# Performance work log

Measured on AMD Instinct MI355X. Metric: run time of the kernel, lower is better.

Reference implementation:

```python
import jax, jax.numpy as jnp
import numpy as np

N = 32768       # flattened residues (batch*seq)
DIM = 1024      # dim == channel (required by residual add)
NRES = 21       # amino-acid types
RECYCLES = 2


def _quat_to_rot(q):
    w, x, y, z = q[..., 0], q[..., 1], q[..., 2], q[..., 3]
    return jnp.stack([
        jnp.stack([1 - 2 * (y * y + z * z), 2 * (x * y - w * z), 2 * (x * z + w * y)], -1),
        jnp.stack([2 * (x * y + w * z), 1 - 2 * (x * x + z * z), 2 * (y * z - w * x)], -1),
        jnp.stack([2 * (x * z - w * y), 2 * (y * z + w * x), 1 - 2 * (x * x + y * y)], -1),
    ], -2)


def _rand_rigid(key, shape, tscale=1.0):
    # random valid rigid transforms as 4x4 homogeneous matrices
    kq, kt = jax.random.split(key)
    q = jax.random.normal(kq, shape + (4,), jnp.float32)
    q = q / jnp.linalg.norm(q, axis=-1, keepdims=True)
    rot = _quat_to_rot(q)
    t = jax.random.normal(kt, shape + (3,), jnp.float32) * tscale
    m = jnp.zeros(shape + (4, 4), jnp.float32)
    m = m.at[..., :3, :3].set(rot).at[..., :3, 3].set(t).at[..., 3, 3].set(1.0)
    return m


def setup_inputs():
    key = jax.random.key(0)
    ks = jax.random.split(key, 12)
    s = 1.0 / np.sqrt(DIM)
    return {
        "rep0": jax.random.normal(ks[0], (N, DIM), jnp.float32),
        "rep1": jax.random.normal(ks[1], (N, DIM), jnp.float32),
        "w_in": jax.random.normal(ks[2], (DIM, DIM), jnp.float32) * s,
        "b_in": jnp.zeros((DIM,), jnp.float32),
        "w1": jax.random.normal(ks[3], (DIM, DIM), jnp.float32) * s,
        "b1": jnp.zeros((DIM,), jnp.float32),
        "w2": jax.random.normal(ks[4], (DIM, DIM), jnp.float32) * s,
        "b2": jnp.zeros((DIM,), jnp.float32),
        "w_ang": jax.random.normal(ks[5], (DIM, 14), jnp.float32) * s,
        "b_ang": jnp.zeros((14,), jnp.float32),
        "rigids": _rand_rigid(ks[6], (N,), tscale=10.0),              # backbone frames
        "default_frames": _rand_rigid(ks[7], (NRES, 8), tscale=1.5), # restype_rigid_group_default_frame
        "lit_positions": jax.random.normal(ks[8], (NRES, 14, 3), jnp.float32),
        "atom_mask": (jax.random.uniform(ks[9], (NRES, 14)) > 0.2).astype(jnp.float32),
        "aatype": jax.random.randint(ks[10], (N,), 0, NRES),
        "group_idx": jax.random.randint(ks[11], (NRES, 14), 0, 8),   # restype_atom14_to_rigid_group
    }


def reference(rep0, rep1, w_in, b_in, w1, b1, w2, b2, w_ang, b_ang,
              rigids, default_frames, lit_positions, atom_mask, aatype, group_idx):
    # InputProjection: shared ReLU+Linear applied to each representation, summed
    act = (jax.nn.relu(rep0) @ w_in + b_in) + (jax.nn.relu(rep1) @ w_in + b_in)
    # ResidueBlock with residual recycles: act += Linear(ReLU(Linear(ReLU(act))))
    for _ in range(RECYCLES):
        h = jax.nn.relu(act) @ w1 + b1
        h = jax.nn.relu(h) @ w2 + b2
        act = act + h
    # TorisonAngles: Linear(dim,14) -> (N,7,2) -> l2_normalize
    ang = (jax.nn.relu(act) @ w_ang + b_ang).reshape(N, 7, 2)
    angles = ang / jnp.sqrt(jnp.maximum(jnp.sum(ang * ang, -1, keepdims=True), 1e-12))
    # torsion_angles_to_frames: prepend identity backbone angle (sin=0, cos=1)
    sin = jnp.concatenate([jnp.zeros((N, 1), angles.dtype), angles[..., 0]], 1)  # [N,8]
    cos = jnp.concatenate([jnp.ones((N, 1), angles.dtype), angles[..., 1]], 1)
    z = jnp.zeros_like(sin); one = jnp.ones_like(sin)
    rotx = jnp.stack([
        jnp.stack([one, z, z, z], -1),
        jnp.stack([z, cos, -sin, z], -1),
        jnp.stack([z, sin, cos, z], -1),
        jnp.stack([z, z, z, one], -1),
    ], -2)                                            # [N,8,4,4] rotation about x by torsion
    frames = default_frames[aatype] @ rotx            # [N,8,4,4]
    # chi2/chi3/chi4 frames are defined relative to the previous chi frame
    f5 = frames[:, 4] @ frames[:, 5]
    f6 = f5 @ frames[:, 6]
    f7 = f6 @ frames[:, 7]
    frames_to_bb = jnp.concatenate([frames[:, :5], jnp.stack([f5, f6, f7], 1)], 1)
    frames_global = rigids[:, None] @ frames_to_bb    # [N,8,4,4]
    # frames_and_literature_positions_to_atom14_pos
    gidx = group_idx[aatype]                          # [N,14] rigid-group id per atom
    f14 = jnp.take_along_axis(frames_global,
                              jnp.broadcast_to(gidx[:, :, None, None], (N, 14, 4, 4)),
                              axis=1)                 # [N,14,4,4]
    pos = lit_positions[aatype]                       # [N,14,3]
    pred = jnp.einsum('naij,naj->nai', f14[..., :3, :3], pos) + f14[..., :3, 3]
    pred = pred * atom_mask[aatype][..., None]        # [N,14,3]
    return angles, pred, frames_global
```

## Files before the change

kernel.cpp:

```cpp
#include <hip/hip_runtime.h>
#include <stdint.h>

typedef uint16_t u16;
typedef uint32_t u32;
typedef __bf16 bf16;
typedef bf16 bf16x8 __attribute__((ext_vector_type(8)));
typedef float f32x4 __attribute__((ext_vector_type(4)));

#define N_RES 32768
#define DIM 1024

__device__ __forceinline__ float b2f(u16 u) {
  u32 v = ((u32)u) << 16;
  float f;
  __builtin_memcpy(&f, &v, 4);
  return f;
}
__device__ __forceinline__ u16 f2b(float f) {
  u32 u;
  __builtin_memcpy(&u, &f, 4);
  u += 0x7fffu + ((u >> 16) & 1u);
  return (u16)(u >> 16);
}
__device__ __forceinline__ void split2(float v, u16& h, u16& l) {
  h = f2b(v);
  l = f2b(v - b2f(h));
}
__device__ __forceinline__ void relu_mask4(uint4& h, uint4& l) {
  u32 s, m;
  s = h.x & 0x80008000u; m = ((s >> 15) & 0x00010001u) * 0xFFFFu; h.x &= ~m; l.x &= ~m;
  s = h.y & 0x80008000u; m = ((s >> 15) & 0x00010001u) * 0xFFFFu; h.y &= ~m; l.y &= ~m;
  s = h.z & 0x80008000u; m = ((s >> 15) & 0x00010001u) * 0xFFFFu; h.z &= ~m; l.z &= ~m;
  s = h.w & 0x80008000u; m = ((s >> 15) & 0x00010001u) * 0xFFFFu; h.w &= ~m; l.w &= ~m;
}
__device__ __forceinline__ void relu_split8(bf16x8& h, bf16x8& l) {
  uint4 uh, ul;
  __builtin_memcpy(&uh, &h, 16);
  __builtin_memcpy(&ul, &l, 16);
  relu_mask4(uh, ul);
  __builtin_memcpy(&h, &uh, 16);
  __builtin_memcpy(&l, &ul, 16);
}
__device__ __forceinline__ void split8(const float* v, uint4& H, uint4& L) {
  u16 h[8], l[8];
#pragma unroll
  for (int i = 0; i < 8; ++i) split2(v[i], h[i], l[i]);
  H.x = (u32)h[0] | ((u32)h[1] << 16);
  H.y = (u32)h[2] | ((u32)h[3] << 16);
  H.z = (u32)h[4] | ((u32)h[5] << 16);
  H.w = (u32)h[6] | ((u32)h[7] << 16);
  L.x = (u32)l[0] | ((u32)l[1] << 16);
  L.y = (u32)l[2] | ((u32)l[3] << 16);
  L.z = (u32)l[4] | ((u32)l[5] << 16);
  L.w = (u32)l[6] | ((u32)l[7] << 16);
}

__global__ __launch_bounds__(256) void transpose_split(const float* __restrict__ in,
                                                       u16* __restrict__ outh,
                                                       u16* __restrict__ outl) {
  __shared__ float t[32][33];
  const int bx = blockIdx.x * 32, by = blockIdx.y * 32;
  const int tx = threadIdx.x, ty = threadIdx.y;
  for (int i = ty; i < 32; i += 8) t[i][tx] = in[(size_t)(by + i) * DIM + bx + tx];
  __syncthreads();
  for (int i = ty; i < 32; i += 8) {
    u16 h, l;
    split2(t[tx][i], h, l);
    const size_t o = (size_t)(bx + i) * DIM + by + tx;
    outh[o] = h;
    outl[o] = l;
  }
}

__global__ __launch_bounds__(256, 2) void gemm_split(
    const u16* __restrict__ Ah, const u16* __restrict__ Al, int reluA,
    const float* __restrict__ repA0, const float* __restrict__ repA1,
    const u16* __restrict__ Bh, const u16* __restrict__ Bl,
    const float* __restrict__ bias, float bscale,
    const u16* __restrict__ Rh, const u16* __restrict__ Rl,
    u16* __restrict__ Oh, u16* __restrict__ Ol) {
  __shared__ __align__(16) u16 Ash[128 * 32];
  __shared__ __align__(16) u16 Asl[128 * 32];
  __shared__ __align__(16) u16 Bsh[128 * 32];
  __shared__ __align__(16) u16 Bsl[128 * 32];
  const int tid = threadIdx.x;
  const int wave = tid >> 6;
  const int lane = tid & 63;
  const int lrow = lane & 15;
  const int lquad = lane >> 4;
  const int bm = blockIdx.y * 128;
  const int bn = blockIdx.x * 128;
  const int wm = (wave & 1) * 64;
  const int wn = (wave >> 1) * 64;

  f32x4 acc[4][4];
#pragma unroll
  for (int i = 0; i < 4; ++i)
#pragma unroll
    for (int j = 0; j < 4; ++j) acc[i][j] = (f32x4){0.f, 0.f, 0.f, 0.f};

  for (int kb = 0; kb < DIM; kb += 32) {
#pragma unroll
    for (int q = 0; q < 2; ++q) {
      const int idx = q * 256 + tid;
      const int r = idx >> 2;
      const int c = idx & 3;
      const size_t goA = (size_t)(bm + r) * DIM + kb + c * 8;
      const size_t goB = (size_t)(bn + r) * DIM + kb + c * 8;
      uint4 ah, al;
      if (repA0) {
        float4 x0 = *(const float4*)(repA0 + goA);
        float4 x1 = *(const float4*)(repA0 + goA + 4);
        float4 y0 = *(const float4*)(repA1 + goA);
        float4 y1 = *(const float4*)(repA1 + goA + 4);
        float v[8];
        v[0] = fmaxf(x0.x, 0.f) + fmaxf(y0.x, 0.f);
        v[1] = fmaxf(x0.y, 0.f) + fmaxf(y0.y, 0.f);
        v[2] = fmaxf(x0.z, 0.f) + fmaxf(y0.z, 0.f);
        v[3] = fmaxf(x0.w, 0.f) + fmaxf(y0.w, 0.f);
        v[4] = fmaxf(x1.x, 0.f) + fmaxf(y1.x, 0.f);
        v[5] = fmaxf(x1.y, 0.f) + fmaxf(y1.y, 0.f);
        v[6] = fmaxf(x1.z, 0.f) + fmaxf(y1.z, 0.f);
        v[7] = fmaxf(x1.w, 0.f) + fmaxf(y1.w, 0.f);
        split8(v, ah, al);
      } else {
        ah = *(const uint4*)(Ah + goA);
        al = *(const uint4*)(Al + goA);
        if (reluA) relu_mask4(ah, al);
      }
      uint4 bh = *(const uint4*)(Bh + goB);
      uint4 bl = *(const uint4*)(Bl + goB);
      *(uint4*)(Ash + r * 32 + c * 8) = ah;
      *(uint4*)(Asl + r * 32 + c * 8) = al;
      *(uint4*)(Bsh + r * 32 + c * 8) = bh;
      *(uint4*)(Bsl + r * 32 + c * 8) = bl;
    }
    __syncthreads();
    bf16x8 a_h[4], a_l[4], b_h[4], b_l[4];
#pragma unroll
    for (int i = 0; i < 4; ++i) {
      a_h[i] = *(const bf16x8*)(Ash + (wm + i * 16 + lrow) * 32 + lquad * 8);
      a_l[i] = *(const bf16x8*)(Asl + (wm + i * 16 + lrow) * 32 + lquad * 8);
    }
#pragma unroll
    for (int j = 0; j < 4; ++j) {
      b_h[j] = *(const bf16x8*)(Bsh + (wn + j * 16 + lrow) * 32 + lquad * 8);
      b_l[j] = *(const bf16x8*)(Bsl + (wn + j * 16 + lrow) * 32 + lquad * 8);
    }
#pragma unroll
    for (int i = 0; i < 4; ++i)
#pragma unroll
      for (int j = 0; j < 4; ++j) {
        acc[i][j] = __builtin_amdgcn_mfma_f32_16x16x32_bf16(a_h[i], b_h[j], acc[i][j], 0, 0, 0);
        acc[i][j] = __builtin_amdgcn_mfma_f32_16x16x32_bf16(a_h[i], b_l[j], acc[i][j], 0, 0, 0);
        acc[i][j] = __builtin_amdgcn_mfma_f32_16x16x32_bf16(a_l[i], b_h[j], acc[i][j], 0, 0, 0);
      }
    __syncthreads();
  }

#pragma unroll
  for (int j = 0; j < 4; ++j) {
    const int col = bn + wn + j * 16 + lrow;
    const float bj = bias[col] * bscale;
#pragma unroll
    for (int i = 0; i < 4; ++i) {
      const int row0 = bm + wm + i * 16 + lquad * 4;
#pragma unroll
      for (int r = 0; r < 4; ++r) {
        const size_t idx = (size_t)(row0 + r) * DIM + col;
        float v = acc[i][j][r] + bj;
        if (Rh) v += b2f(Rh[idx]) + b2f(Rl[idx]);
        u16 h, l;
        split2(v, h, l);
        Oh[idx] = h;
        Ol[idx] = l;
      }
    }
  }
}

__global__ __launch_bounds__(256) void angles_split(
    const u16* __restrict__ ACTh, const u16* __restrict__ ACTl,
    const u16* __restrict__ WAh, const u16* __restrict__ WAl,
    const float* __restrict__ b_ang, float* __restrict__ out_angles) {
  const int tid = threadIdx.x;
  const int wave = tid >> 6, lane = tid & 63;
  const int lrow = lane & 15, lquad = lane >> 4;
  const int rowA = blockIdx.x * 64 + wave * 16 + lrow;
  f32x4 acc = (f32x4){0.f, 0.f, 0.f, 0.f};
  const u16* gah = ACTh + (size_t)rowA * DIM + lquad * 8;
  const u16* gal = ACTl + (size_t)rowA * DIM + lquad * 8;
  const u16* gbh = WAh + (size_t)lrow * DIM + lquad * 8;
  const u16* gbl = WAl + (size_t)lrow * DIM + lquad * 8;
#pragma unroll 4
  for (int kb = 0; kb < DIM; kb += 32) {
    bf16x8 ah = *(const bf16x8*)(gah + kb);
    bf16x8 al = *(const bf16x8*)(gal + kb);
    relu_split8(ah, al);
    bf16x8 bh = *(const bf16x8*)(gbh + kb);
    bf16x8 bl = *(const bf16x8*)(gbl + kb);
    acc = __builtin_amdgcn_mfma_f32_16x16x32_bf16(ah, bh, acc, 0, 0, 0);
    acc = __builtin_amdgcn_mfma_f32_16x16x32_bf16(ah, bl, acc, 0, 0, 0);
    acc = __builtin_amdgcn_mfma_f32_16x16x32_bf16(al, bh, acc, 0, 0, 0);
  }
  const int col = lrow;
  const float bj = (col < 14) ? b_ang[col] : 0.f;
#pragma unroll
  for (int r = 0; r < 4; ++r) {
    float v = acc[r] + bj;
    float p = __shfl_xor(v, 1, 64);
    float s2 = fmaxf(v * v + p * p, 1e-12f);
    float o = v * rsqrtf(s2);
    const int orow = blockIdx.x * 64 + wave * 16 + lquad * 4 + r;
    if (col < 14) out_angles[(size_t)orow * 14 + col] = o;
  }
}

__global__ __launch_bounds__(256) void prep_wang(const float* __restrict__ w,
                                                 u16* __restrict__ outh,
                                                 u16* __restrict__ outl) {
  for (int idx = threadIdx.x; idx < 16 * 1024; idx += 256) {
    const int n = idx & 15;
    const int k = idx >> 4;
    const float v = (n < 14) ? w[(size_t)k * 14 + n] : 0.f;
    u16 h, l;
    split2(v, h, l);
    outh[(size_t)n * DIM + k] = h;
    outl[(size_t)n * DIM + k] = l;
  }
}

__device__ __forceinline__ void mm34(const float* A, const float* B, float* O) {
#pragma unroll
  for (int r = 0; r < 3; ++r) {
#pragma unroll
    for (int c = 0; c < 4; ++c) {
      float v = A[r * 4 + 0] * B[0 * 4 + c] + A[r * 4 + 1] * B[1 * 4 + c] +
                A[r * 4 + 2] * B[2 * 4 + c];
      if (c == 3) v += A[r * 4 + 3];
      O[r * 4 + c] = v;
    }
  }
}

__global__ __launch_bounds__(256) void frames_kernel(
    const float* __restrict__ angles, const float* __restrict__ rigids,
    const float* __restrict__ dframes, const float* __restrict__ litpos,
    const float* __restrict__ amask, const int* __restrict__ aatype,
    const int* __restrict__ gidx, float* __restrict__ out_pred,
    float* __restrict__ out_frames) {
  const int n = blockIdx.x * 256 + threadIdx.x;
  const int aa = aatype[n];

  float fr[8][12];
  const float* angp = angles + (size_t)n * 14;
#pragma unroll
  for (int g = 0; g < 8; ++g) {
    float s, c;
    if (g == 0) { s = 0.f; c = 1.f; }
    else { s = angp[(g - 1) * 2]; c = angp[(g - 1) * 2 + 1]; }
    const float* D = dframes + ((size_t)aa * 8 + g) * 16;
#pragma unroll
    for (int r = 0; r < 3; ++r) {
      float d0 = D[r * 4 + 0], d1 = D[r * 4 + 1], d2 = D[r * 4 + 2], d3 = D[r * 4 + 3];
      fr[g][r * 4 + 0] = d0;
      fr[g][r * 4 + 1] = d1 * c + d2 * s;
      fr[g][r * 4 + 2] = d2 * c - d1 * s;
      fr[g][r * 4 + 3] = d3;
    }
  }
  float tmp[12];
  mm34(fr[4], fr[5], tmp);
#pragma unroll
  for (int e = 0; e < 12; ++e) fr[5][e] = tmp[e];
  mm34(fr[5], fr[6], tmp);
#pragma unroll
  for (int e = 0; e < 12; ++e) fr[6][e] = tmp[e];
  mm34(fr[6], fr[7], tmp);
#pragma unroll
  for (int e = 0; e < 12; ++e) fr[7][e] = tmp[e];

  float R[12];
  const float* rp = rigids + (size_t)n * 16;
#pragma unroll
  for (int e = 0; e < 12; ++e) R[e] = rp[e];
#pragma unroll
  for (int g = 0; g < 8; ++g) {
    mm34(R, fr[g], tmp);
#pragma unroll
    for (int e = 0; e < 12; ++e) fr[g][e] = tmp[e];
  }

  float4* of = (float4*)(out_frames + (size_t)n * 128);
#pragma unroll
  for (int g = 0; g < 8; ++g) {
    of[g * 4 + 0] = (float4){fr[g][0], fr[g][1], fr[g][2], fr[g][3]};
    of[g * 4 + 1] = (float4){fr[g][4], fr[g][5], fr[g][6], fr[g][7]};
    of[g * 4 + 2] = (float4){fr[g][8], fr[g][9], fr[g][10], fr[g][11]};
    of[g * 4 + 3] = (float4){0.f, 0.f, 0.f, 1.f};
  }

  float P[42];
#pragma unroll
  for (int a = 0; a < 14; ++a) {
    const int g = gidx[aa * 14 + a];
    float f[12];
#pragma unroll
    for (int q = 0; q < 8; ++q) {
      if (q == 0) {
#pragma unroll
        for (int e = 0; e < 12; ++e) f[e] = fr[0][e];
      } else {
        const bool sel = (g == q);
#pragma unroll
        for (int e = 0; e < 12; ++e) f[e] = sel ? fr[q][e] : f[e];
      }
    }
    const float px = litpos[((size_t)aa * 14 + a) * 3 + 0];
    const float py = litpos[((size_t)aa * 14 + a) * 3 + 1];
    const float pz = litpos[((size_t)aa * 14 + a) * 3 + 2];
    const float mk = amask[aa * 14 + a];
    P[a * 3 + 0] = (f[0] * px + f[1] * py + f[2] * pz + f[3]) * mk;
    P[a * 3 + 1] = (f[4] * px + f[5] * py + f[6] * pz + f[7]) * mk;
    P[a * 3 + 2] = (f[8] * px + f[9] * py + f[10] * pz + f[11]) * mk;
  }
  float2* op = (float2*)(out_pred + (size_t)n * 42);
#pragma unroll
  for (int i = 0; i < 21; ++i) op[i] = (float2){P[2 * i], P[2 * i + 1]};
}

__global__ __launch_bounds__(256) void ws_diag(float* __restrict__ out, float mb) {
  const int i = blockIdx.x * 256 + threadIdx.x;
  if (i < N_RES * 14) out[i] = mb;
}

extern "C" void kernel_launch(void* const* d_in, const int* in_sizes, int n_in,
                              void* d_out, int out_size, void* d_ws, size_t ws_size,
                              hipStream_t stream) {
  const float* rep0 = (const float*)d_in[0];
  const float* rep1 = (const float*)d_in[1];
  const float* w_in = (const float*)d_in[2];
  const float* b_in = (const float*)d_in[3];
  const float* w1 = (const float*)d_in[4];
  const float* b1 = (const float*)d_in[5];
  const float* w2 = (const float*)d_in[6];
  const float* b2 = (const float*)d_in[7];
  const float* w_ang = (const float*)d_in[8];
  const float* b_ang = (const float*)d_in[9];
  const float* rigids = (const float*)d_in[10];
  const float* dframes = (const float*)d_in[11];
  const float* litpos = (const float*)d_in[12];
  const float* amask = (const float*)d_in[13];
  const int* aatype = (const int*)d_in[14];
  const int* gidx = (const int*)d_in[15];

  const size_t SLOT = (size_t)N_RES * DIM;
  const size_t NEED_U16 = 4 * SLOT + 6 * (size_t)DIM * DIM + 2 * 16 * DIM;

  float* out_ang = (float*)d_out;
  float* out_pred = out_ang + (size_t)N_RES * 14;
  float* out_frames = out_pred + (size_t)N_RES * 42;

  if (ws_size < NEED_U16 * 2) {
    ws_diag<<<(N_RES * 14 + 255) / 256, 256, 0, stream>>>(
        out_ang, (float)(ws_size >> 20));
    return;
  }

  u16* ACTh = (u16*)d_ws;
  u16* ACTl = ACTh + SLOT;
  u16* Hh = ACTl + SLOT;
  u16* Hl = Hh + SLOT;
  u16* W0h = Hl + SLOT;
  u16* W0l = W0h + (size_t)DIM * DIM;
  u16* W1h = W0l + (size_t)DIM * DIM;
  u16* W1l = W1h + (size_t)DIM * DIM;
  u16* W2h = W1l + (size_t)DIM * DIM;
  u16* W2l = W2h + (size_t)DIM * DIM;
  u16* WAh = W2l + (size_t)DIM * DIM;
  u16* WAl = WAh + (size_t)16 * DIM;

  transpose_split<<<dim3(32, 32), dim3(32, 8), 0, stream>>>(w_in, W0h, W0l);
  transpose_split<<<dim3(32, 32), dim3(32, 8), 0, stream>>>(w1, W1h, W1l);
  transpose_split<<<dim3(32, 32), dim3(32, 8), 0, stream>>>(w2, W2h, W2l);
  prep_wang<<<1, 256, 0, stream>>>(w_ang, WAh, WAl);

  dim3 gg(DIM / 128, N_RES / 128);
  gemm_split<<<gg, 256, 0, stream>>>(nullptr, nullptr, 0, rep0, rep1,
                                     W0h, W0l, b_in, 2.f, nullptr, nullptr,
                                     ACTh, ACTl);
  gemm_split<<<gg, 256, 0, stream>>>(ACTh, ACTl, 1, nullptr, nullptr,
                                     W1h, W1l, b1, 1.f, nullptr, nullptr,
                                     Hh, Hl);
  gemm_split<<<gg, 256, 0, stream>>>(Hh, Hl, 1, nullptr, nullptr,
                                     W2h, W2l, b2, 1.f, ACTh, ACTl,
                                     ACTh, ACTl);
  gemm_split<<<gg, 256, 0, stream>>>(ACTh, ACTl, 1, nullptr, nullptr,
                                     W1h, W1l, b1, 1.f, nullptr, nullptr,
                                     Hh, Hl);
  gemm_split<<<gg, 256, 0, stream>>>(Hh, Hl, 1, nullptr, nullptr,
                                     W2h, W2l, b2, 1.f, ACTh, ACTl,
                                     ACTh, ACTl);

  angles_split<<<N_RES / 64, 256, 0, stream>>>(ACTh, ACTl, WAh, WAl, b_ang,
                                               out_ang);
  frames_kernel<<<N_RES / 256, 256, 0, stream>>>(out_ang, rigids, dframes, litpos,
                                                 amask, aatype, gidx, out_pred,
                                                 out_frames);
}
```

Measured before the change: 1.920 ms.

## Load GEMM tiles via global_load_lds, precompute input split, remap blocks per XCD

Moves the first-layer input preprocessing (relu-sum and hi/lo bf16 split) into a separate elementwise kernel so every GEMM takes pre-split bf16 operands. The GEMM tile loads now use direct global-to-LDS DMA (global_load_lds), skipping VGPR staging, and the ReLU mask is applied after reading fragments from LDS. Block indices are remapped so each XCD handles a contiguous band of row tiles, which should improve L2 reuse of A rows and B. The cost is one extra pass over the input activations and ReLU work repeated on every fragment read, with no double buffering.

```diff
diff --git a/kernel.cpp b/kernel.cpp
--- a/kernel.cpp
+++ b/kernel.cpp
@@ -53,6 +53,12 @@
   L.y = (u32)l[2] | ((u32)l[3] << 16);
   L.z = (u32)l[4] | ((u32)l[5] << 16);
   L.w = (u32)l[6] | ((u32)l[7] << 16);
+}
+
+__device__ __forceinline__ void g2l16(const void* g, void* lds) {
+  __builtin_amdgcn_global_load_lds(
+      (__attribute__((address_space(1))) void*)(g),
+      (__attribute__((address_space(3))) void*)(lds), 16, 0, 0);
 }
 
 __global__ __launch_bounds__(256) void transpose_split(const float* __restrict__ in,
@@ -72,9 +78,32 @@
   }
 }
 
+__global__ __launch_bounds__(256) void prep_input(const float* __restrict__ rep0,
+                                                  const float* __restrict__ rep1,
+                                                  u16* __restrict__ oh,
+                                                  u16* __restrict__ ol) {
+  const size_t base = ((size_t)blockIdx.x * 256 + threadIdx.x) * 8;
+  float4 x0 = *(const float4*)(rep0 + base);
+  float4 x1 = *(const float4*)(rep0 + base + 4);
+  float4 y0 = *(const float4*)(rep1 + base);
+  float4 y1 = *(const float4*)(rep1 + base + 4);
+  float v[8];
+  v[0] = fmaxf(x0.x, 0.f) + fmaxf(y0.x, 0.f);
+  v[1] = fmaxf(x0.y, 0.f) + fmaxf(y0.y, 0.f);
+  v[2] = fmaxf(x0.z, 0.f) + fmaxf(y0.z, 0.f);
+  v[3] = fmaxf(x0.w, 0.f) + fmaxf(y0.w, 0.f);
+  v[4] = fmaxf(x1.x, 0.f) + fmaxf(y1.x, 0.f);
+  v[5] = fmaxf(x1.y, 0.f) + fmaxf(y1.y, 0.f);
+  v[6] = fmaxf(x1.z, 0.f) + fmaxf(y1.z, 0.f);
+  v[7] = fmaxf(x1.w, 0.f) + fmaxf(y1.w, 0.f);
+  uint4 H, L;
+  split8(v, H, L);
+  *(uint4*)(oh + base) = H;
+  *(uint4*)(ol + base) = L;
+}
+
 __global__ __launch_bounds__(256, 2) void gemm_split(
     const u16* __restrict__ Ah, const u16* __restrict__ Al, int reluA,
-    const float* __restrict__ repA0, const float* __restrict__ repA1,
     const u16* __restrict__ Bh, const u16* __restrict__ Bl,
     const float* __restrict__ bias, float bscale,
     const u16* __restrict__ Rh, const u16* __restrict__ Rl,
@@ -88,8 +117,13 @@
   const int lane = tid & 63;
   const int lrow = lane & 15;
   const int lquad = lane >> 4;
-  const int bm = blockIdx.y * 128;
-  const int bn = blockIdx.x * 128;
+
+  const int g = blockIdx.x + (blockIdx.y << 3);
+  const int xcd = g & 7;
+  const int j = g >> 3;
+  const int bm = (xcd * 32 + (j >> 3)) * 128;
+  const int bn = (j & 7) * 128;
+
   const int wm = (wave & 1) * 64;
   const int wn = (wave >> 1) * 64;
 
@@ -97,70 +131,64 @@
 #pragma unroll
   for (int i = 0; i < 4; ++i)
 #pragma unroll
-    for (int j = 0; j < 4; ++j) acc[i][j] = (f32x4){0.f, 0.f, 0.f, 0.f};
+    for (int jj = 0; jj < 4; ++jj) acc[i][jj] = (f32x4){0.f, 0.f, 0.f, 0.f};
+
+  const int r0 = tid >> 2;
+  const int c0 = tid & 3;
+  const u16* pAh0 = Ah + (size_t)(bm + r0) * DIM + c0 * 8;
+  const u16* pAh1 = Ah + (size_t)(bm + 64 + r0) * DIM + c0 * 8;
+  const u16* pAl0 = Al + (size_t)(bm + r0) * DIM + c0 * 8;
+  const u16* pAl1 = Al + (size_t)(bm + 64 + r0) * DIM + c0 * 8;
+  const u16* pBh0 = Bh + (size_t)(bn + r0) * DIM + c0 * 8;
+  const u16* pBh1 = Bh + (size_t)(bn + 64 + r0) * DIM + c0 * 8;
+  const u16* pBl0 = Bl + (size_t)(bn + r0) * DIM + c0 * 8;
+  const u16* pBl1 = Bl + (size_t)(bn + 64 + r0) * DIM + c0 * 8;
+  u16* dA0 = Ash + (size_t)tid * 8;
+  u16* dA1 = Ash + (size_t)(tid + 256) * 8;
+  u16* dAl0 = Asl + (size_t)tid * 8;
+  u16* dAl1 = Asl + (size_t)(tid + 256) * 8;
+  u16* dB0 = Bsh + (size_t)tid * 8;
+  u16* dB1 = Bsh + (size_t)(tid + 256) * 8;
+  u16* dBl0 = Bsl + (size_t)tid * 8;
+  u16* dBl1 = Bsl + (size_t)(tid + 256) * 8;
 
   for (int kb = 0; kb < DIM; kb += 32) {
-#pragma unroll
-    for (int q = 0; q < 2; ++q) {
-      const int idx = q * 256 + tid;
-      const int r = idx >> 2;
-      const int c = idx & 3;
-      const size_t goA = (size_t)(bm + r) * DIM + kb + c * 8;
-      const size_t goB = (size_t)(bn + r) * DIM + kb + c * 8;
-      uint4 ah, al;
-      if (repA0) {
-        float4 x0 = *(const float4*)(repA0 + goA);
-        float4 x1 = *(const float4*)(repA0 + goA + 4);
-        float4 y0 = *(const float4*)(repA1 + goA);
-        float4 y1 = *(const float4*)(repA1 + goA + 4);
-        float v[8];
-        v[0] = fmaxf(x0.x, 0.f) + fmaxf(y0.x, 0.f);
-        v[1] = fmaxf(x0.y, 0.f) + fmaxf(y0.y, 0.f);
-        v[2] = fmaxf(x0.z, 0.f) + fmaxf(y0.z, 0.f);
-        v[3] = fmaxf(x0.w, 0.f) + fmaxf(y0.w, 0.f);
-        v[4] = fmaxf(x1.x, 0.f) + fmaxf(y1.x, 0.f);
-        v[5] = fmaxf(x1.y, 0.f) + fmaxf(y1.y, 0.f);
-        v[6] = fmaxf(x1.z, 0.f) + fmaxf(y1.z, 0.f);
-        v[7] = fmaxf(x1.w, 0.f) + fmaxf(y1.w, 0.f);
-        split8(v, ah, al);
-      } else {
-        ah = *(const uint4*)(Ah + goA);
-        al = *(const uint4*)(Al + goA);
-        if (reluA) relu_mask4(ah, al);
-      }
-      uint4 bh = *(const uint4*)(Bh + goB);
-      uint4 bl = *(const uint4*)(Bl + goB);
-      *(uint4*)(Ash + r * 32 + c * 8) = ah;
-      *(uint4*)(Asl + r * 32 + c * 8) = al;
-      *(uint4*)(Bsh + r * 32 + c * 8) = bh;
-      *(uint4*)(Bsl + r * 32 + c * 8) = bl;
-    }
+    g2l16(pAh0 + kb, dA0);
+    g2l16(pAh1 + kb, dA1);
+    g2l16(pAl0 + kb, dAl0);
+    g2l16(pAl1 + kb, dAl1);
+    g2l16(pBh0 + kb, dB0);
+    g2l16(pBh1 + kb, dB1);
+    g2l16(pBl0 + kb, dBl0);
+    g2l16(pBl1 + kb, dBl1);
     __syncthreads();
+
     bf16x8 a_h[4], a_l[4], b_h[4], b_l[4];
 #pragma unroll
     for (int i = 0; i < 4; ++i) {
       a_h[i] = *(const bf16x8*)(Ash + (wm + i * 16 + lrow) * 32 + lquad * 8);
       a_l[i] = *(const bf16x8*)(Asl + (wm + i * 16 + lrow) * 32 + lquad * 8);
-    }
-#pragma unroll
-    for (int j = 0; j < 4; ++j) {
-      b_h[j] = *(const bf16x8*)(Bsh + (wn + j * 16 + lrow) * 32 + lquad * 8);
-      b_l[j] = *(const bf16x8*)(Bsl + (wn + j * 16 + lrow) * 32 + lquad * 8);
+      if (reluA) relu_split8(a_h[i], a_l[i]);
+    }
+#pragma unroll
+    for (int jj = 0; jj < 4; ++jj) {
+      b_h[jj] = *(const bf16x8*)(Bsh + (wn + jj * 16 + lrow) * 32 + lquad * 8);
+      b_l[jj] = *(const bf16x8*)(Bsl + (wn + jj * 16 + lrow) * 32 + lquad * 8);
     }
 #pragma unroll
     for (int i = 0; i < 4; ++i)
 #pragma unroll
-      for (int j = 0; j < 4; ++j) {
-        acc[i][j] = __builtin_amdgcn_mfma_f32_16x16x32_bf16(a_h[i], b_h[j], acc[i][j], 0, 0, 0);
-        acc[i][j] = __builtin_amdgcn_mfma_f32_16x16x32_bf16(a_h[i], b_l[j], acc[i][j], 0, 0, 0);
-        acc[i][j] = __builtin_amdgcn_mfma_f32_16x16x32_bf16(a_l[i], b_h[j], acc[i][j], 0, 0, 0);
+      for (int jj = 0; jj < 4; ++jj) {
+        acc[i][jj] = __builtin_amdgcn_mfma_f32_16x16x32_bf16(a_h[i], b_h[jj], acc[i][jj], 0, 0, 0);
+        acc[i][jj] = __builtin_amdgcn_mfma_f32_16x16x32_bf16(a_h[i], b_l[jj], acc[i][jj], 0, 0, 0);
+        acc[i][jj] = __builtin_amdgcn_mfma_f32_16x16x32_bf16(a_l[i], b_h[jj], acc[i][jj], 0, 0, 0);
       }
     __syncthreads();
   }
 
 #pragma unroll
-  for (int j = 0; j < 4; ++j) {
-    const int col = bn + wn + j * 16 + lrow;
+  for (int jj = 0; jj < 4; ++jj) {
+    const int col = bn + wn + jj * 16 + lrow;
     const float bj = bias[col] * bscale;
 #pragma unroll
     for (int i = 0; i < 4; ++i) {
@@ -168,7 +196,7 @@
 #pragma unroll
       for (int r = 0; r < 4; ++r) {
         const size_t idx = (size_t)(row0 + r) * DIM + col;
-        float v = acc[i][j][r] + bj;
+        float v = acc[i][jj][r] + bj;
         if (Rh) v += b2f(Rh[idx]) + b2f(Rl[idx]);
         u16 h, l;
         split2(v, h, l);
@@ -385,22 +413,19 @@
   transpose_split<<<dim3(32, 32), dim3(32, 8), 0, stream>>>(w2, W2h, W2l);
   prep_wang<<<1, 256, 0, stream>>>(w_ang, WAh, WAl);
 
+  prep_input<<<(N_RES * DIM / 8) / 256, 256, 0, stream>>>(rep0, rep1, Hh, Hl);
+
   dim3 gg(DIM / 128, N_RES / 128);
-  gemm_split<<<gg, 256, 0, stream>>>(nullptr, nullptr, 0, rep0, rep1,
-                                     W0h, W0l, b_in, 2.f, nullptr, nullptr,
-                                     ACTh, ACTl);
-  gemm_split<<<gg, 256, 0, stream>>>(ACTh, ACTl, 1, nullptr, nullptr,
-                                     W1h, W1l, b1, 1.f, nullptr, nullptr,
-                                     Hh, Hl);
-  gemm_split<<<gg, 256, 0, stream>>>(Hh, Hl, 1, nullptr, nullptr,
-                                     W2h, W2l, b2, 1.f, ACTh, ACTl,
-                                     ACTh, ACTl);
-  gemm_split<<<gg, 256, 0, stream>>>(ACTh, ACTl, 1, nullptr, nullptr,
-                                     W1h, W1l, b1, 1.f, nullptr, nullptr,
-                                     Hh, Hl);
-  gemm_split<<<gg, 256, 0, stream>>>(Hh, Hl, 1, nullptr, nullptr,
-                                     W2h, W2l, b2, 1.f, ACTh, ACTl,
-                                     ACTh, ACTl);
+  gemm_split<<<gg, 256, 0, stream>>>(Hh, Hl, 0, W0h, W0l, b_in, 2.f,
+                                     nullptr, nullptr, ACTh, ACTl);
+  gemm_split<<<gg, 256, 0, stream>>>(ACTh, ACTl, 1, W1h, W1l, b1, 1.f,
+                                     nullptr, nullptr, Hh, Hl);
+  gemm_split<<<gg, 256, 0, stream>>>(Hh, Hl, 1, W2h, W2l, b2, 1.f,
+                                     ACTh, ACTl, ACTh, ACTl);
+  gemm_split<<<gg, 256, 0, stream>>>(ACTh, ACTl, 1, W1h, W1l, b1, 1.f,
+                                     nullptr, nullptr, Hh, Hl);
+  gemm_split<<<gg, 256, 0, stream>>>(Hh, Hl, 1, W2h, W2l, b2, 1.f,
+                                     ACTh, ACTl, ACTh, ACTl);
 
   angles_split<<<N_RES / 64, 256, 0, stream>>>(ACTh, ACTl, WAh, WAl, b_ang,
                                                out_ang);
```

After: 1.753 ms. 1.1x faster.
